# Kernel tuning notes

Hardware: AMD Instinct MI355X
Metric: run time of the kernel (lower is better)

The kernel has to match this reference:

```python
import jax, jax.numpy as jnp
import numpy as np

N_HEAD, D_MODEL, D_K, D_V = 8, 512, 64, 64
B, S = 4, 2048
LN_EPS = 1e-5


def setup_inputs() -> dict:
    key = jax.random.key(0)
    ks = jax.random.split(key, 12)
    std_qk = np.sqrt(2.0 / (D_MODEL + D_K))
    std_v = np.sqrt(2.0 / (D_MODEL + D_V))
    return {
        "q": jax.random.normal(ks[0], (B, S, D_MODEL), jnp.float32),
        "k": jax.random.normal(ks[1], (B, S, D_MODEL), jnp.float32),
        "v": jax.random.normal(ks[2], (B, S, D_MODEL), jnp.float32),
        "w_qs": jax.random.normal(ks[3], (N_HEAD * D_K, D_MODEL), jnp.float32) * std_qk,
        "b_qs": jnp.zeros((N_HEAD * D_K,), jnp.float32),
        "w_ks": jax.random.normal(ks[4], (N_HEAD * D_K, D_MODEL), jnp.float32) * std_qk,
        "b_ks": jnp.zeros((N_HEAD * D_K,), jnp.float32),
        "w_vs": jax.random.normal(ks[5], (N_HEAD * D_V, D_MODEL), jnp.float32) * std_v,
        "b_vs": jnp.zeros((N_HEAD * D_V,), jnp.float32),
        "w_fc": jax.random.normal(ks[6], (D_MODEL, N_HEAD * D_V), jnp.float32) * np.sqrt(2.0 / (D_MODEL + N_HEAD * D_V)),
        "b_fc": jnp.zeros((D_MODEL,), jnp.float32),
        "ln_g": jnp.ones((D_MODEL,), jnp.float32),
        "ln_b": jnp.zeros((D_MODEL,), jnp.float32),
    }


def reference(q, k, v, w_qs, b_qs, w_ks, b_ks, w_vs, b_vs, w_fc, b_fc, ln_g, ln_b):
    sz_b, len_q, _ = q.shape
    residual = q
    temperature = np.power(D_K, 0.5).astype(np.float32)
    # Projections: [b, s, h*dk] -> [h, b, s, dk]  (matches permute(2,0,1,3))
    qh = (jnp.einsum('bsd,fd->bsf', q, w_qs) + b_qs).reshape(sz_b, len_q, N_HEAD, D_K).transpose(2, 0, 1, 3)
    kh = (jnp.einsum('bsd,fd->bsf', k, w_ks) + b_ks).reshape(sz_b, -1, N_HEAD, D_K).transpose(2, 0, 1, 3)
    vh = (jnp.einsum('bsd,fd->bsf', v, w_vs) + b_vs).reshape(sz_b, -1, N_HEAD, D_V).transpose(2, 0, 1, 3)
    # Scaled dot-product attention (dropout is identity in eval)
    attn = jnp.einsum('hbqd,hbkd->hbqk', qh, kh) / temperature
    attn = jax.nn.softmax(attn, axis=-1)
    out = jnp.einsum('hbqk,hbkv->hbqv', attn, vh)          # [h, b, q, dv]
    out = out.transpose(1, 2, 0, 3).reshape(sz_b, len_q, N_HEAD * D_V)
    out = jnp.einsum('bsf,df->bsd', out, w_fc) + b_fc
    # Residual + LayerNorm
    x = out + residual
    mu = jnp.mean(x, axis=-1, keepdims=True)
    var = jnp.mean(jnp.square(x - mu), axis=-1, keepdims=True)
    x = (x - mu) * jax.lax.rsqrt(var + LN_EPS) * ln_g + ln_b
    # attn returned as [(n_head*b), len_q, len_k] to match torch bmm layout
    return x, attn.reshape(N_HEAD * sz_b, len_q, -1)
```

## Files before the change

### kernel.cpp

```cpp
#include <hip/hip_runtime.h>
#include <hip/hip_bf16.h>

constexpr int NB  = 4;
constexpr int NS  = 2048;
constexpr int NH  = 8;
constexpr int DM  = 512;
constexpr int DKV = 64;
constexpr int HB  = NH * NB;

typedef __attribute__((ext_vector_type(8))) short short8;
typedef __attribute__((ext_vector_type(4))) short short4v;
typedef __attribute__((ext_vector_type(4))) float f32x4;

__device__ inline unsigned short f2bf(float f) {
    unsigned u = __builtin_bit_cast(unsigned, f);
    u = (u + 0x7fffu + ((u >> 16) & 1u)) >> 16;
    return (unsigned short)u;
}
__device__ inline float bf2f(unsigned short h) {
    unsigned u = ((unsigned)h) << 16;
    return __builtin_bit_cast(float, u);
}
__device__ inline short8 ld8(const unsigned short* p) { return *(const short8*)p; }

__device__ inline short8 pack8(const float* p) {
    f32x4 a = *(const f32x4*)p;
    f32x4 b = *(const f32x4*)(p + 4);
    short8 r;
    r[0] = (short)f2bf(a[0]); r[1] = (short)f2bf(a[1]);
    r[2] = (short)f2bf(a[2]); r[3] = (short)f2bf(a[3]);
    r[4] = (short)f2bf(b[0]); r[5] = (short)f2bf(b[1]);
    r[6] = (short)f2bf(b[2]); r[7] = (short)f2bf(b[3]);
    return r;
}

__device__ inline f32x4 mfma16(short8 a, short8 b, f32x4 c) {
    return __builtin_amdgcn_mfma_f32_16x16x32_bf16(a, b, c, 0, 0, 0);
}

__device__ inline void gl_lds16(const void* g, void* l) {
    __builtin_amdgcn_global_load_lds(
        (const __attribute__((address_space(1))) unsigned*)g,
        (__attribute__((address_space(3))) unsigned*)l, 16, 0, 0);
}

__device__ inline void bar() { __builtin_amdgcn_s_barrier(); }

__global__ __launch_bounds__(256) void k_cvtw(const float* __restrict__ s0,
                                              const float* __restrict__ s1,
                                              const float* __restrict__ s2,
                                              const float* __restrict__ s3,
                                              unsigned short* __restrict__ d0,
                                              unsigned short* __restrict__ d1,
                                              unsigned short* __restrict__ d2,
                                              unsigned short* __restrict__ d3)
{
    const float* s; unsigned short* d;
    switch (blockIdx.y) {
        case 0:  s = s0; d = d0; break;
        case 1:  s = s1; d = d1; break;
        case 2:  s = s2; d = d2; break;
        default: s = s3; d = d3; break;
    }
    const size_t i = ((size_t)blockIdx.x * 256 + threadIdx.x) * 8;
    *(short8*)(d + i) = pack8(s + i);
}

__global__ __launch_bounds__(256, 4) void k_proj3(const float* __restrict__ Xq,
                                                  const float* __restrict__ Xk,
                                                  const float* __restrict__ Xv,
                                                  const unsigned short* __restrict__ Wq,
                                                  const unsigned short* __restrict__ Wk,
                                                  const unsigned short* __restrict__ Wv,
                                                  const float* __restrict__ bq,
                                                  const float* __restrict__ bk,
                                                  const float* __restrict__ bv,
                                                  unsigned short* __restrict__ oq,
                                                  unsigned short* __restrict__ ok,
                                                  unsigned short* __restrict__ ov)
{
    const float* X; const unsigned short* W; const float* bias; unsigned short* out;
    float scale = 1.0f; int vtrans = 0;
    switch (blockIdx.z) {
        case 0:  X = Xq; W = Wq; bias = bq; out = oq;
                 scale = 0.125f * 1.44269504088896340736f; break;
        case 1:  X = Xk; W = Wk; bias = bk; out = ok; break;
        default: X = Xv; W = Wv; bias = bv; out = ov; vtrans = 1; break;
    }
    const int tid = threadIdx.x;
    const int l = tid & 63, w = tid >> 6;
    const int c = l & 15, g = l >> 4;
    const int m0 = blockIdx.y * 64 + w * 16;
    const int f0 = blockIdx.x * 64;
    const int arow = m0 + c;

    f32x4 acc[4] = {};
    const float* aB = X + (size_t)arow * DM;
    for (int kb = 0; kb < DM; kb += 32) {
        short8 af = pack8(aB + kb + g * 8);
#pragma unroll
        for (int n = 0; n < 4; ++n) {
            short8 bf = ld8(W + (size_t)(f0 + n * 16 + c) * DM + kb + g * 8);
            acc[n] = mfma16(af, bf, acc[n]);
        }
    }
#pragma unroll
    for (int n = 0; n < 4; ++n) {
        const int f = f0 + n * 16 + c;
        const int h = f >> 6, d = f & 63;
        const float bvv = bias[f];
#pragma unroll
        for (int r = 0; r < 4; ++r) {
            const int m = m0 + g * 4 + r;
            const int bb = m >> 11, s = m & (NS - 1);
            const int hb = h * NB + bb;
            const float v = (acc[n][r] + bvv) * scale;
            const size_t idx = vtrans ? ((size_t)(hb * DKV + d) * NS + s)
                                      : ((size_t)(hb * NS + s) * DKV + d);
            out[idx] = f2bf(v);
        }
    }
}

__global__ __launch_bounds__(256, 4) void k_attn(const unsigned short* __restrict__ Qh,
                                                 const unsigned short* __restrict__ Kh,
                                                 const unsigned short* __restrict__ Vt,
                                                 float* __restrict__ attn,
                                                 unsigned short* __restrict__ Obuf)
{
    __shared__ __align__(16) char kld[2][8192];
    __shared__ __align__(16) char vld[2][8192];
    __shared__ __align__(16) char plds[4 * 2048];
    const int tid = threadIdx.x;
    const int l = tid & 63, w = tid >> 6;
    const int c = l & 15, g = l >> 4;
    constexpr int NT = NS / 64;

    const int bid = blockIdx.x;
    const int wid = (bid & 7) * 128 + (bid >> 3);
    const int hb = wid >> 5;
    const int q0 = (wid & 31) * 64 + w * 16;
    char* myp = plds + w * 2048;

    const char* kbytes = (const char*)(Kh + (size_t)hb * NS * DKV);
    const char* vbytes = (const char*)(Vt + (size_t)hb * DKV * NS);

    const unsigned short* qb = Qh + ((size_t)hb * NS + q0 + c) * DKV + g * 8;
    const short8 qf0 = ld8(qb), qf1 = ld8(qb + 32);

    int koff[2], voff[2];
#pragma unroll
    for (int j = 0; j < 2; ++j) {
        const int D = (w * 2 + j) * 1024 + l * 16;
        const int row = D >> 7;
        const int scolb = (D & 127) ^ ((row & 7) << 4);
        koff[j] = row * 128 + scolb;
        voff[j] = row * (NS * 2) + scolb;
    }
    const int swc = (c & 7) << 4;

    const int ldsbase = w * 2048;

    float ls = 0.f;
    {
        gl_lds16(kbytes + koff[0], kld[0] + ldsbase);
        gl_lds16(kbytes + koff[1], kld[0] + ldsbase + 1024);
        asm volatile("s_waitcnt vmcnt(0)" ::: "memory");
        bar();
        __builtin_amdgcn_sched_barrier(0);
        int cur = 0;
        for (int kt = 0; kt < NT; ++kt) {
            if (kt + 1 < NT) {
                const size_t nb = (size_t)(kt + 1) * 64 * 128;
                gl_lds16(kbytes + nb + koff[0], kld[cur ^ 1] + ldsbase);
                gl_lds16(kbytes + nb + koff[1], kld[cur ^ 1] + ldsbase + 1024);
            }
            if (kt > 0) {
                if (kt + 1 < NT) { asm volatile("s_waitcnt vmcnt(2)" ::: "memory"); }
                else             { asm volatile("s_waitcnt vmcnt(0)" ::: "memory"); }
                bar();
                __builtin_amdgcn_sched_barrier(0);
            }
#pragma unroll
            for (int t = 0; t < 4; ++t) {
                const int rb = (t * 16 + c) * 128;
                const short8 b0 = *(const short8*)(kld[cur] + rb + ((g * 16) ^ swc));
                const short8 b1 = *(const short8*)(kld[cur] + rb + ((64 + g * 16) ^ swc));
                f32x4 z = {};
                z = mfma16(b0, qf0, z);
                z = mfma16(b1, qf1, z);
#pragma unroll
                for (int r = 0; r < 4; ++r) ls += exp2f(z[r]);
            }
            bar();
            cur ^= 1;
        }
    }
    ls += __shfl_xor(ls, 16);
    ls += __shfl_xor(ls, 32);
    const float li = 1.0f / ls;

    f32x4 oacc[4] = {};
    float* arow = attn + (size_t)hb * NS * NS + (size_t)(q0 + c) * NS + g * 4;

    {
        gl_lds16(kbytes + koff[0], kld[0] + ldsbase);
        gl_lds16(kbytes + koff[1], kld[0] + ldsbase + 1024);
        gl_lds16(vbytes + voff[0], vld[0] + ldsbase);
        gl_lds16(vbytes + voff[1], vld[0] + ldsbase + 1024);
        asm volatile("s_waitcnt vmcnt(0)" ::: "memory");
        bar();
        __builtin_amdgcn_sched_barrier(0);
        int cur = 0;
        for (int kt = 0; kt < NT; ++kt) {
            const int k0 = kt * 64;
            if (kt + 1 < NT) {
                const size_t nkb = (size_t)(k0 + 64) * 128;
                const size_t nvb = (size_t)(k0 + 64) * 2;
                gl_lds16(kbytes + nkb + koff[0], kld[cur ^ 1] + ldsbase);
                gl_lds16(kbytes + nkb + koff[1], kld[cur ^ 1] + ldsbase + 1024);
                gl_lds16(vbytes + nvb + voff[0], vld[cur ^ 1] + ldsbase);
                gl_lds16(vbytes + nvb + voff[1], vld[cur ^ 1] + ldsbase + 1024);
            }
            if (kt > 0) {
                if (kt + 1 < NT) { asm volatile("s_waitcnt vmcnt(8)" ::: "memory"); }
                else             { asm volatile("s_waitcnt vmcnt(4)" ::: "memory"); }
                bar();
                __builtin_amdgcn_sched_barrier(0);
            }
            f32x4 sc[4];
#pragma unroll
            for (int t = 0; t < 4; ++t) {
                const int rb = (t * 16 + c) * 128;
                const short8 b0 = *(const short8*)(kld[cur] + rb + ((g * 16) ^ swc));
                const short8 b1 = *(const short8*)(kld[cur] + rb + ((64 + g * 16) ^ swc));
                f32x4 z = {};
                z = mfma16(b0, qf0, z);
                z = mfma16(b1, qf1, z);
                sc[t] = z;
            }
#pragma unroll
            for (int t = 0; t < 4; ++t) {
                f32x4 pv;
#pragma unroll
                for (int r = 0; r < 4; ++r) pv[r] = exp2f(sc[t][r]) * li;
                *(f32x4*)(arow + k0 + t * 16) = pv;
                short4v pk;
                pk[0] = (short)f2bf(pv[0]); pk[1] = (short)f2bf(pv[1]);
                pk[2] = (short)f2bf(pv[2]); pk[3] = (short)f2bf(pv[3]);
                *(short4v*)(myp + c * 128 + ((t * 32 + g * 8) ^ swc)) = pk;
            }
            asm volatile("s_waitcnt lgkmcnt(0)" ::: "memory");
            __builtin_amdgcn_sched_barrier(0);
#pragma unroll
            for (int kk = 0; kk < 2; ++kk) {
                const short8 pa = *(const short8*)(myp + c * 128 + ((kk * 64 + g * 16) ^ swc));
#pragma unroll
                for (int n = 0; n < 4; ++n) {
                    const int rb = (n * 16 + c) * 128;
                    const short8 vb = *(const short8*)(vld[cur] + rb + ((kk * 64 + g * 16) ^ swc));
                    oacc[n] = mfma16(pa, vb, oacc[n]);
                }
            }
            bar();
            cur ^= 1;
        }
    }

    const int h = hb >> 2, bb = hb & 3;
#pragma unroll
    for (int n = 0; n < 4; ++n)
#pragma unroll
        for (int r = 0; r < 4; ++r) {
            const int q = q0 + g * 4 + r;
            const int dv = n * 16 + c;
            Obuf[((size_t)(bb * NS + q)) * DM + h * DKV + dv] = f2bf(oacc[n][r]);
        }
}

__global__ __launch_bounds__(256, 4) void k_fc(const unsigned short* __restrict__ O,
                                            const unsigned short* __restrict__ Wfc,
                                            const float* __restrict__ bfc,
                                            const float* __restrict__ resid,
                                            unsigned short* __restrict__ Y)
{
    const int tid = threadIdx.x;
    const int l = tid & 63, w = tid >> 6;
    const int c = l & 15, g = l >> 4;
    const int m0 = blockIdx.y * 64 + w * 16;
    const int f0 = blockIdx.x * 64;
    const int arow = m0 + c;

    f32x4 acc[4] = {};
    const unsigned short* aB = O + (size_t)arow * DM;
    for (int kb = 0; kb < DM; kb += 32) {
        short8 af = ld8(aB + kb + g * 8);
#pragma unroll
        for (int n = 0; n < 4; ++n) {
            short8 bf = ld8(Wfc + (size_t)(f0 + n * 16 + c) * DM + kb + g * 8);
            acc[n] = mfma16(af, bf, acc[n]);
        }
    }
#pragma unroll
    for (int n = 0; n < 4; ++n) {
        const int d = f0 + n * 16 + c;
        const float bv = bfc[d];
#pragma unroll
        for (int r = 0; r < 4; ++r) {
            const int m = m0 + g * 4 + r;
            const float v = acc[n][r] + bv + resid[(size_t)m * DM + d];
            Y[(size_t)m * DM + d] = f2bf(v);
        }
    }
}

__global__ __launch_bounds__(256) void k_ln(const unsigned short* __restrict__ Y,
                                            const float* __restrict__ gam,
                                            const float* __restrict__ bet,
                                            float* __restrict__ out)
{
    const int tid = threadIdx.x;
    const int l = tid & 63, w = tid >> 6;
    const int row = blockIdx.x * 4 + w;

    const short8 yv = ld8(Y + (size_t)row * DM + l * 8);
    float x[8];
#pragma unroll
    for (int j = 0; j < 8; ++j) x[j] = bf2f((unsigned short)yv[j]);

    float s = 0.f;
#pragma unroll
    for (int j = 0; j < 8; ++j) s += x[j];
#pragma unroll
    for (int mask = 1; mask <= 32; mask <<= 1) s += __shfl_xor(s, mask);
    const float mean = s * (1.0f / DM);

    float d2 = 0.f;
#pragma unroll
    for (int j = 0; j < 8; ++j) { const float t = x[j] - mean; d2 += t * t; }
#pragma unroll
    for (int mask = 1; mask <= 32; mask <<= 1) d2 += __shfl_xor(d2, mask);
    const float rstd = rsqrtf(d2 * (1.0f / DM) + 1e-5f);

#pragma unroll
    for (int j = 0; j < 8; ++j) {
        const int d = l * 8 + j;
        out[(size_t)row * DM + d] = (x[j] - mean) * rstd * gam[d] + bet[d];
    }
}

extern "C" void kernel_launch(void* const* d_in, const int* in_sizes, int n_in,
                              void* d_out, int out_size, void* d_ws, size_t ws_size,
                              hipStream_t stream)
{
    const float* q    = (const float*)d_in[0];
    const float* k    = (const float*)d_in[1];
    const float* v    = (const float*)d_in[2];
    const float* w_qs = (const float*)d_in[3];
    const float* b_qs = (const float*)d_in[4];
    const float* w_ks = (const float*)d_in[5];
    const float* b_ks = (const float*)d_in[6];
    const float* w_vs = (const float*)d_in[7];
    const float* b_vs = (const float*)d_in[8];
    const float* w_fc = (const float*)d_in[9];
    const float* b_fc = (const float*)d_in[10];
    const float* ln_g = (const float*)d_in[11];
    const float* ln_b = (const float*)d_in[12];

    char* ws = (char*)d_ws;
    unsigned short* Qh = (unsigned short*)(ws);
    unsigned short* Kh = (unsigned short*)(ws + (8u  << 20));
    unsigned short* Vt = (unsigned short*)(ws + (16u << 20));
    unsigned short* Ob = (unsigned short*)(ws + (24u << 20));
    unsigned short* Yb = (unsigned short*)(ws + (32u << 20));
    unsigned short* Wq = (unsigned short*)(ws + (40u << 20));
    unsigned short* Wk = Wq + (size_t)DM * DM;
    unsigned short* Wv = Wk + (size_t)DM * DM;
    unsigned short* Wf = Wv + (size_t)DM * DM;

    float* xout = (float*)d_out;
    float* attn = xout + (size_t)NB * NS * DM;

    k_cvtw<<<dim3(128, 4), 256, 0, stream>>>(w_qs, w_ks, w_vs, w_fc, Wq, Wk, Wv, Wf);

    k_proj3<<<dim3(8, 128, 3), 256, 0, stream>>>(q, k, v, Wq, Wk, Wv,
                                                 b_qs, b_ks, b_vs, Qh, Kh, Vt);

    k_attn<<<1024, 256, 0, stream>>>(Qh, Kh, Vt, attn, Ob);

    k_fc<<<dim3(8, 128), 256, 0, stream>>>(Ob, Wf, b_fc, q, Yb);
    k_ln<<<NB * NS / 4, 256, 0, stream>>>(Yb, ln_g, ln_b, xout);
}
```

Baseline: 404.7 us.

## Split softmax denominator pass into separate split-K kernel before attention

Moves the first pass, which computes the row sums of exp of scores, out of the attention kernel into its own kernel. That kernel splits the key range into two halves across twice as many blocks and writes partial sums to workspace, and the attention kernel adds the two partials. The aim is more parallelism and less serial latency in the sum pass, plus a lighter attention kernel. The cost is an extra launch and a small workspace round trip.

```diff
diff --git a/kernel.cpp b/kernel.cpp
--- a/kernel.cpp
+++ b/kernel.cpp
@@ -122,43 +122,36 @@
     }
 }
 
-__global__ __launch_bounds__(256, 4) void k_attn(const unsigned short* __restrict__ Qh,
-                                                 const unsigned short* __restrict__ Kh,
-                                                 const unsigned short* __restrict__ Vt,
-                                                 float* __restrict__ attn,
-                                                 unsigned short* __restrict__ Obuf)
+__global__ __launch_bounds__(256, 4) void k_sum(const unsigned short* __restrict__ Qh,
+                                                const unsigned short* __restrict__ Kh,
+                                                float* __restrict__ Lp)
 {
     __shared__ __align__(16) char kld[2][8192];
-    __shared__ __align__(16) char vld[2][8192];
-    __shared__ __align__(16) char plds[4 * 2048];
     const int tid = threadIdx.x;
     const int l = tid & 63, w = tid >> 6;
     const int c = l & 15, g = l >> 4;
-    constexpr int NT = NS / 64;
 
     const int bid = blockIdx.x;
-    const int wid = (bid & 7) * 128 + (bid >> 3);
-    const int hb = wid >> 5;
-    const int q0 = (wid & 31) * 64 + w * 16;
-    char* myp = plds + w * 2048;
-
-    const char* kbytes = (const char*)(Kh + (size_t)hb * NS * DKV);
-    const char* vbytes = (const char*)(Vt + (size_t)hb * DKV * NS);
+    const int wid = (bid & 7) * 256 + (bid >> 3);
+    const int hb = wid >> 6;
+    const int rem = wid & 63;
+    const int q0 = (rem >> 1) * 64 + w * 16;
+    const int ks = rem & 1;
+
+    const char* kbytes = (const char*)(Kh + ((size_t)hb * NS + ks * 1024) * DKV);
 
     const unsigned short* qb = Qh + ((size_t)hb * NS + q0 + c) * DKV + g * 8;
     const short8 qf0 = ld8(qb), qf1 = ld8(qb + 32);
 
-    int koff[2], voff[2];
+    int koff[2];
 #pragma unroll
     for (int j = 0; j < 2; ++j) {
         const int D = (w * 2 + j) * 1024 + l * 16;
         const int row = D >> 7;
         const int scolb = (D & 127) ^ ((row & 7) << 4);
         koff[j] = row * 128 + scolb;
-        voff[j] = row * (NS * 2) + scolb;
     }
     const int swc = (c & 7) << 4;
-
     const int ldsbase = w * 2048;
 
     float ls = 0.f;
@@ -169,14 +162,14 @@
         bar();
         __builtin_amdgcn_sched_barrier(0);
         int cur = 0;
-        for (int kt = 0; kt < NT; ++kt) {
-            if (kt + 1 < NT) {
-                const size_t nb = (size_t)(kt + 1) * 64 * 128;
+        for (int kt = 0; kt < 16; ++kt) {
+            if (kt + 1 < 16) {
+                const size_t nb = (size_t)(kt + 1) * 8192;
                 gl_lds16(kbytes + nb + koff[0], kld[cur ^ 1] + ldsbase);
                 gl_lds16(kbytes + nb + koff[1], kld[cur ^ 1] + ldsbase + 1024);
             }
             if (kt > 0) {
-                if (kt + 1 < NT) { asm volatile("s_waitcnt vmcnt(2)" ::: "memory"); }
+                if (kt + 1 < 16) { asm volatile("s_waitcnt vmcnt(2)" ::: "memory"); }
                 else             { asm volatile("s_waitcnt vmcnt(0)" ::: "memory"); }
                 bar();
                 __builtin_amdgcn_sched_barrier(0);
@@ -198,7 +191,50 @@
     }
     ls += __shfl_xor(ls, 16);
     ls += __shfl_xor(ls, 32);
-    const float li = 1.0f / ls;
+    if (l < 16) Lp[(size_t)ks * HB * NS + hb * NS + q0 + l] = ls;
+}
+
+__global__ __launch_bounds__(256, 4) void k_att(const unsigned short* __restrict__ Qh,
+                                                const unsigned short* __restrict__ Kh,
+                                                const unsigned short* __restrict__ Vt,
+                                                const float* __restrict__ Lp,
+                                                float* __restrict__ attn,
+                                                unsigned short* __restrict__ Obuf)
+{
+    __shared__ __align__(16) char kld[2][8192];
+    __shared__ __align__(16) char vld[2][8192];
+    __shared__ __align__(16) char plds[4 * 2048];
+    const int tid = threadIdx.x;
+    const int l = tid & 63, w = tid >> 6;
+    const int c = l & 15, g = l >> 4;
+    constexpr int NT = NS / 64;
+
+    const int bid = blockIdx.x;
+    const int wid = (bid & 7) * 128 + (bid >> 3);
+    const int hb = wid >> 5;
+    const int q0 = (wid & 31) * 64 + w * 16;
+    char* myp = plds + w * 2048;
+
+    const char* kbytes = (const char*)(Kh + (size_t)hb * NS * DKV);
+    const char* vbytes = (const char*)(Vt + (size_t)hb * DKV * NS);
+
+    const unsigned short* qb = Qh + ((size_t)hb * NS + q0 + c) * DKV + g * 8;
+    const short8 qf0 = ld8(qb), qf1 = ld8(qb + 32);
+
+    int koff[2], voff[2];
+#pragma unroll
+    for (int j = 0; j < 2; ++j) {
+        const int D = (w * 2 + j) * 1024 + l * 16;
+        const int row = D >> 7;
+        const int scolb = (D & 127) ^ ((row & 7) << 4);
+        koff[j] = row * 128 + scolb;
+        voff[j] = row * (NS * 2) + scolb;
+    }
+    const int swc = (c & 7) << 4;
+    const int ldsbase = w * 2048;
+
+    const size_t lidx = (size_t)hb * NS + q0 + c;
+    const float li = 1.0f / (Lp[lidx] + Lp[(size_t)HB * NS + lidx]);
 
     f32x4 oacc[4] = {};
     float* arow = attn + (size_t)hb * NS * NS + (size_t)(q0 + c) * NS + g * 4;
@@ -377,6 +413,7 @@
     unsigned short* Wk = Wq + (size_t)DM * DM;
     unsigned short* Wv = Wk + (size_t)DM * DM;
     unsigned short* Wf = Wv + (size_t)DM * DM;
+    float*          Lpart = (float*)(ws + (48u << 20));
 
     float* xout = (float*)d_out;
     float* attn = xout + (size_t)NB * NS * DM;
@@ -386,7 +423,8 @@
     k_proj3<<<dim3(8, 128, 3), 256, 0, stream>>>(q, k, v, Wq, Wk, Wv,
                                                  b_qs, b_ks, b_vs, Qh, Kh, Vt);
 
-    k_attn<<<1024, 256, 0, stream>>>(Qh, Kh, Vt, attn, Ob);
+    k_sum<<<2048, 256, 0, stream>>>(Qh, Kh, Lpart);
+    k_att<<<1024, 256, 0, stream>>>(Qh, Kh, Vt, Lpart, attn, Ob);
 
     k_fc<<<dim3(8, 128), 256, 0, stream>>>(Ob, Wf, b_fc, q, Yb);
     k_ln<<<NB * NS / 4, 256, 0, stream>>>(Yb, ln_g, ln_b, xout);
```

After: 411.8 us. Within noise of the previous version (+1.8%).

## Switch attention kernel to 32x32 MFMA tiles with 32 queries per wave

Applied to the files above, without the earlier changes.

The attention kernel moves from 16x16x32 bf16 MFMA to 32x32x16 bf16 MFMA, and each wave now handles 32 query rows instead of 16. Each block covers 128 queries, so the grid halves and every K/V tile staged in LDS is reused across twice as many queries. This cuts K/V global traffic and LDS reads per FLOP. In exchange it needs more registers per thread, larger P staging in LDS and lower occupancy (launch bounds 3). The large attention-matrix write, which likely dominates, is unchanged.

```diff
diff --git a/kernel.cpp b/kernel.cpp
--- a/kernel.cpp
+++ b/kernel.cpp
@@ -11,6 +11,7 @@
 typedef __attribute__((ext_vector_type(8))) short short8;
 typedef __attribute__((ext_vector_type(4))) short short4v;
 typedef __attribute__((ext_vector_type(4))) float f32x4;
+typedef __attribute__((ext_vector_type(16))) float f32x16;
 
 __device__ inline unsigned short f2bf(float f) {
     unsigned u = __builtin_bit_cast(unsigned, f);
@@ -36,6 +37,9 @@
 
 __device__ inline f32x4 mfma16(short8 a, short8 b, f32x4 c) {
     return __builtin_amdgcn_mfma_f32_16x16x32_bf16(a, b, c, 0, 0, 0);
+}
+__device__ inline f32x16 mfma32(short8 a, short8 b, f32x16 c) {
+    return __builtin_amdgcn_mfma_f32_32x32x16_bf16(a, b, c, 0, 0, 0);
 }
 
 __device__ inline void gl_lds16(const void* g, void* l) {
@@ -122,7 +126,7 @@
     }
 }
 
-__global__ __launch_bounds__(256, 4) void k_attn(const unsigned short* __restrict__ Qh,
+__global__ __launch_bounds__(256, 3) void k_attn(const unsigned short* __restrict__ Qh,
                                                  const unsigned short* __restrict__ Kh,
                                                  const unsigned short* __restrict__ Vt,
                                                  float* __restrict__ attn,
@@ -130,23 +134,26 @@
 {
     __shared__ __align__(16) char kld[2][8192];
     __shared__ __align__(16) char vld[2][8192];
-    __shared__ __align__(16) char plds[4 * 2048];
+    __shared__ __align__(16) char plds[4 * 4096];
     const int tid = threadIdx.x;
     const int l = tid & 63, w = tid >> 6;
-    const int c = l & 15, g = l >> 4;
+    const int l31 = l & 31, hi = l >> 5;
+    const int sw = (l & 7) << 4;
     constexpr int NT = NS / 64;
 
     const int bid = blockIdx.x;
-    const int wid = (bid & 7) * 128 + (bid >> 3);
-    const int hb = wid >> 5;
-    const int q0 = (wid & 31) * 64 + w * 16;
-    char* myp = plds + w * 2048;
+    const int wid = (bid & 7) * 64 + (bid >> 3);
+    const int hb = wid >> 4;
+    const int q0 = (wid & 15) * 128 + w * 32;
+    char* myp = plds + w * 4096;
 
     const char* kbytes = (const char*)(Kh + (size_t)hb * NS * DKV);
     const char* vbytes = (const char*)(Vt + (size_t)hb * DKV * NS);
 
-    const unsigned short* qb = Qh + ((size_t)hb * NS + q0 + c) * DKV + g * 8;
-    const short8 qf0 = ld8(qb), qf1 = ld8(qb + 32);
+    short8 qf[4];
+#pragma unroll
+    for (int ds = 0; ds < 4; ++ds)
+        qf[ds] = ld8(Qh + ((size_t)hb * NS + q0 + l31) * DKV + ds * 16 + hi * 8);
 
     int koff[2], voff[2];
 #pragma unroll
@@ -157,8 +164,6 @@
         koff[j] = row * 128 + scolb;
         voff[j] = row * (NS * 2) + scolb;
     }
-    const int swc = (c & 7) << 4;
-
     const int ldsbase = w * 2048;
 
     float ls = 0.f;
@@ -171,7 +176,7 @@
         int cur = 0;
         for (int kt = 0; kt < NT; ++kt) {
             if (kt + 1 < NT) {
-                const size_t nb = (size_t)(kt + 1) * 64 * 128;
+                const size_t nb = (size_t)(kt + 1) * 8192;
                 gl_lds16(kbytes + nb + koff[0], kld[cur ^ 1] + ldsbase);
                 gl_lds16(kbytes + nb + koff[1], kld[cur ^ 1] + ldsbase + 1024);
             }
@@ -182,26 +187,26 @@
                 __builtin_amdgcn_sched_barrier(0);
             }
 #pragma unroll
-            for (int t = 0; t < 4; ++t) {
-                const int rb = (t * 16 + c) * 128;
-                const short8 b0 = *(const short8*)(kld[cur] + rb + ((g * 16) ^ swc));
-                const short8 b1 = *(const short8*)(kld[cur] + rb + ((64 + g * 16) ^ swc));
-                f32x4 z = {};
-                z = mfma16(b0, qf0, z);
-                z = mfma16(b1, qf1, z);
-#pragma unroll
-                for (int r = 0; r < 4; ++r) ls += exp2f(z[r]);
+            for (int ktile = 0; ktile < 2; ++ktile) {
+                f32x16 z = {};
+#pragma unroll
+                for (int ds = 0; ds < 4; ++ds) {
+                    const short8 a = *(const short8*)(kld[cur] + (ktile * 32 + l31) * 128
+                                                      + ((ds * 32 + hi * 16) ^ sw));
+                    z = mfma32(a, qf[ds], z);
+                }
+#pragma unroll
+                for (int r = 0; r < 16; ++r) ls += exp2f(z[r]);
             }
             bar();
             cur ^= 1;
         }
     }
-    ls += __shfl_xor(ls, 16);
     ls += __shfl_xor(ls, 32);
     const float li = 1.0f / ls;
 
-    f32x4 oacc[4] = {};
-    float* arow = attn + (size_t)hb * NS * NS + (size_t)(q0 + c) * NS + g * 4;
+    f32x16 oacc0 = {}, oacc1 = {};
+    float* arow = attn + (size_t)hb * NS * NS + (size_t)(q0 + l31) * NS + 4 * hi;
 
     {
         gl_lds16(kbytes + koff[0], kld[0] + ldsbase);
@@ -223,44 +228,46 @@
                 gl_lds16(vbytes + nvb + voff[1], vld[cur ^ 1] + ldsbase + 1024);
             }
             if (kt > 0) {
-                if (kt + 1 < NT) { asm volatile("s_waitcnt vmcnt(8)" ::: "memory"); }
-                else             { asm volatile("s_waitcnt vmcnt(4)" ::: "memory"); }
+                if (kt + 1 < NT) { asm volatile("s_waitcnt vmcnt(12)" ::: "memory"); }
+                else             { asm volatile("s_waitcnt vmcnt(8)" ::: "memory"); }
                 bar();
                 __builtin_amdgcn_sched_barrier(0);
             }
-            f32x4 sc[4];
-#pragma unroll
-            for (int t = 0; t < 4; ++t) {
-                const int rb = (t * 16 + c) * 128;
-                const short8 b0 = *(const short8*)(kld[cur] + rb + ((g * 16) ^ swc));
-                const short8 b1 = *(const short8*)(kld[cur] + rb + ((64 + g * 16) ^ swc));
-                f32x4 z = {};
-                z = mfma16(b0, qf0, z);
-                z = mfma16(b1, qf1, z);
-                sc[t] = z;
-            }
-#pragma unroll
-            for (int t = 0; t < 4; ++t) {
-                f32x4 pv;
-#pragma unroll
-                for (int r = 0; r < 4; ++r) pv[r] = exp2f(sc[t][r]) * li;
-                *(f32x4*)(arow + k0 + t * 16) = pv;
-                short4v pk;
-                pk[0] = (short)f2bf(pv[0]); pk[1] = (short)f2bf(pv[1]);
-                pk[2] = (short)f2bf(pv[2]); pk[3] = (short)f2bf(pv[3]);
-                *(short4v*)(myp + c * 128 + ((t * 32 + g * 8) ^ swc)) = pk;
-            }
+            f32x16 sc[2];
+#pragma unroll
+            for (int ktile = 0; ktile < 2; ++ktile) {
+                f32x16 z = {};
+#pragma unroll
+                for (int ds = 0; ds < 4; ++ds) {
+                    const short8 a = *(const short8*)(kld[cur] + (ktile * 32 + l31) * 128
+                                                      + ((ds * 32 + hi * 16) ^ sw));
+                    z = mfma32(a, qf[ds], z);
+                }
+                sc[ktile] = z;
+            }
+#pragma unroll
+            for (int ktile = 0; ktile < 2; ++ktile)
+#pragma unroll
+                for (int grp = 0; grp < 4; ++grp) {
+                    f32x4 pv;
+#pragma unroll
+                    for (int j = 0; j < 4; ++j) pv[j] = exp2f(sc[ktile][grp * 4 + j]) * li;
+                    *(f32x4*)(arow + k0 + ktile * 32 + grp * 8) = pv;
+                    short4v pk;
+                    pk[0] = (short)f2bf(pv[0]); pk[1] = (short)f2bf(pv[1]);
+                    pk[2] = (short)f2bf(pv[2]); pk[3] = (short)f2bf(pv[3]);
+                    *(short4v*)(myp + l31 * 128 + ((ktile * 64 + grp * 16 + hi * 8) ^ sw)) = pk;
+                }
             asm volatile("s_waitcnt lgkmcnt(0)" ::: "memory");
             __builtin_amdgcn_sched_barrier(0);
 #pragma unroll
-            for (int kk = 0; kk < 2; ++kk) {
-                const short8 pa = *(const short8*)(myp + c * 128 + ((kk * 64 + g * 16) ^ swc));
-#pragma unroll
-                for (int n = 0; n < 4; ++n) {
-                    const int rb = (n * 16 + c) * 128;
-                    const short8 vb = *(const short8*)(vld[cur] + rb + ((kk * 64 + g * 16) ^ swc));
-                    oacc[n] = mfma16(pa, vb, oacc[n]);
-                }
+            for (int ks = 0; ks < 4; ++ks) {
+                const int kb = (ks * 32 + hi * 16) ^ sw;
+                const short8 pa  = *(const short8*)(myp + l31 * 128 + kb);
+                const short8 vb0 = *(const short8*)(vld[cur] + l31 * 128 + kb);
+                const short8 vb1 = *(const short8*)(vld[cur] + (32 + l31) * 128 + kb);
+                oacc0 = mfma32(pa, vb0, oacc0);
+                oacc1 = mfma32(pa, vb1, oacc1);
             }
             bar();
             cur ^= 1;
@@ -269,13 +276,12 @@
 
     const int h = hb >> 2, bb = hb & 3;
 #pragma unroll
-    for (int n = 0; n < 4; ++n)
-#pragma unroll
-        for (int r = 0; r < 4; ++r) {
-            const int q = q0 + g * 4 + r;
-            const int dv = n * 16 + c;
-            Obuf[((size_t)(bb * NS + q)) * DM + h * DKV + dv] = f2bf(oacc[n][r]);
-        }
+    for (int reg = 0; reg < 16; ++reg) {
+        const int q = q0 + (reg & 3) + 8 * (reg >> 2) + 4 * hi;
+        const size_t base = ((size_t)(bb * NS + q)) * DM + h * DKV;
+        Obuf[base + l31]      = f2bf(oacc0[reg]);
+        Obuf[base + 32 + l31] = f2bf(oacc1[reg]);
+    }
 }
 
 __global__ __launch_bounds__(256, 4) void k_fc(const unsigned short* __restrict__ O,
@@ -386,7 +392,7 @@
     k_proj3<<<dim3(8, 128, 3), 256, 0, stream>>>(q, k, v, Wq, Wk, Wv,
                                                  b_qs, b_ks, b_vs, Qh, Kh, Vt);
 
-    k_attn<<<1024, 256, 0, stream>>>(Qh, Kh, Vt, attn, Ob);
+    k_attn<<<512, 256, 0, stream>>>(Qh, Kh, Vt, attn, Ob);
 
     k_fc<<<dim3(8, 128), 256, 0, stream>>>(Ob, Wf, b_fc, q, Yb);
     k_ln<<<NB * NS / 4, 256, 0, stream>>>(Yb, ln_g, ln_b, xout);
```

Result: no change. 412.6 us (+2.0%).
